# Optimization experiments

Hardware: AMD Instinct MI355X
Metric: run time of the kernel (lower is better)

## Reference

```python
import jax, jax.numpy as jnp
import numpy as np

EPS = 1e-12  # matches torch F.normalize default eps


def _l2norm(x):
    n = jnp.linalg.norm(x, axis=-1, keepdims=True)
    return x / jnp.maximum(n, EPS)


def setup_inputs() -> dict:
    key = jax.random.key(0)
    k1, k2 = jax.random.split(key)
    B, Na, T, Nv, D = 16, 128, 10, 196, 256
    audio_feats = jax.random.normal(k1, (B, Na, D), dtype=jnp.float32)
    visual_feats = jax.random.normal(k2, (B, T, Nv, D), dtype=jnp.float32)
    temperature = jnp.asarray(2.0, dtype=jnp.float32)
    return {"audio_feats": audio_feats, "visual_feats": visual_feats,
            "temperature": temperature}


def reference(audio_feats, visual_feats, temperature):
    # audio_feats: (B, Na, D); visual_feats: (B, T, Nv, D)
    a = _l2norm(audio_feats)                         # (B, Na, D)
    v = _l2norm(visual_feats)                        # (B, T, Nv, D)
    # all-pairs token-level cosine sims: (Bx, By, Na, T, Nv)
    sims = jnp.einsum('xad,ytvd->xyatv', a, v) / temperature
    # aggregate: max over patches, mean over time, mean over audio tokens
    clip_sims = sims.max(axis=-1).mean(axis=-1).mean(axis=-1)  # (B, B)

    # InfoNCE on diagonal
    B = clip_sims.shape[0]
    diag = jnp.arange(B)
    log_p_a2v = jax.nn.log_softmax(clip_sims, axis=1)
    log_p_v2a = jax.nn.log_softmax(clip_sims.T, axis=1)
    losses = -(log_p_a2v[diag, diag] + log_p_v2a[diag, diag])
    contrastive_loss = 0.5 * losses.mean()

    # regularization: non-negativity pressure + temperature band [1, 3]
    neg = jnp.minimum(sims, 0.0)
    l_nonneg = jnp.mean(neg * neg)
    log_t = jnp.log(temperature)
    temp_low = jnp.maximum(-log_t, 0.0) ** 4
    temp_high = jnp.maximum(log_t - jnp.log(3.0), 0.0) ** 4
    reg_loss = l_nonneg + temp_low + temp_high

    total_loss = contrastive_loss + 0.3 * reg_loss
    return (total_loss, contrastive_loss, reg_loss)
```

## Files before the change

### kernel.cpp

```cpp
#include <hip/hip_runtime.h>
#include <stdint.h>


typedef __bf16 bf16x8 __attribute__((ext_vector_type(8)));
typedef float  f32x4  __attribute__((ext_vector_type(4)));

#define P_ROWS 2176

#define WS_A_OFF  ((size_t)0)
#define WS_V_OFF  ((size_t)(1u<<20))
#define WS_CP_OFF (WS_V_OFF + (size_t)16*P_ROWS*512)

__device__ __forceinline__ unsigned short f2bf(float f) {
    unsigned b = __float_as_uint(f);
    return (unsigned short)((b + 0x7fffu + ((b >> 16) & 1u)) >> 16);
}
__device__ __forceinline__ int fenc(float f) {
    int i = __float_as_int(f);
    return i >= 0 ? i : (i ^ 0x7fffffff);
}
__device__ __forceinline__ float fdec(int i) {
    return __int_as_float(i >= 0 ? i : (i ^ 0x7fffffff));
}
__device__ __forceinline__ void gld_lds16(const char* g, char* l) {
    __builtin_amdgcn_global_load_lds(
        (const __attribute__((address_space(1))) void*)g,
        (__attribute__((address_space(3))) void*)l, 16, 0, 0);
}

__global__ __launch_bounds__(512) void prep_kernel(const float* __restrict__ audio,
                                                   const float* __restrict__ visual,
                                                   char* __restrict__ ws)
{
    const int wrow = blockIdx.x * 8 + (threadIdx.x >> 6);
    const int lane = threadIdx.x & 63;
    if (wrow < 2048) {
        const float4 v = *(const float4*)(audio + (size_t)wrow * 256 + lane * 4);
        float ss = v.x*v.x + v.y*v.y + v.z*v.z + v.w*v.w;
        #pragma unroll
        for (int m = 1; m < 64; m <<= 1) ss += __shfl_xor(ss, m);
        const float sc = 1.0f / fmaxf(sqrtf(ss), 1e-12f);
        ushort4 o;
        o.x = f2bf(v.x*sc); o.y = f2bf(v.y*sc); o.z = f2bf(v.z*sc); o.w = f2bf(v.w*sc);
        *(ushort4*)(ws + WS_A_OFF + (size_t)wrow * 512 + lane * 8) = o;
    } else {
        const int vr  = wrow - 2048;
        const int y   = vr / P_ROWS;
        const int rem = vr % P_ROWS;
        const int t   = rem / 208;
        const int v   = rem % 208;
        ushort4 o = make_ushort4(0, 0, 0, 0);
        if (t < 10 && v < 196) {
            const float4 f = *(const float4*)(visual + (size_t)((y*10 + t)*196 + v) * 256 + lane * 4);
            float ss = f.x*f.x + f.y*f.y + f.z*f.z + f.w*f.w;
            #pragma unroll
            for (int m = 1; m < 64; m <<= 1) ss += __shfl_xor(ss, m);
            const float sc = 1.0f / fmaxf(sqrtf(ss), 1e-12f);
            o.x = f2bf(f.x*sc); o.y = f2bf(f.y*sc); o.z = f2bf(f.z*sc); o.w = f2bf(f.w*sc);
        }
        const int u   = lane >> 1;
        const int swz = u ^ (vr & 7);
        *(ushort4*)(ws + WS_V_OFF + (size_t)vr * 512 + (swz << 4) + ((lane & 1) << 3)) = o;
    }
}

#define STAGE(c_, buf_) do {                                        \
    const char* s_ = vbase + (size_t)(c_) * 32768 + tid * 16;       \
    char* d_ = &smem[buf_][0] + tid * 16;                           \
    gld_lds16(s_,         d_);                                      \
    gld_lds16(s_ +  8192, d_ +  8192);                              \
    gld_lds16(s_ + 16384, d_ + 16384);                              \
    gld_lds16(s_ + 24576, d_ + 24576);                              \
} while (0)

__global__ __launch_bounds__(512, 4) void main_kernel(char* __restrict__ ws)
{
    __shared__ __align__(16) char smem[2][32768];
    __shared__ int part_lds[640];
    __shared__ float red[16];

    const int tid  = threadIdx.x;
    const int lane = tid & 63;
    const int wid  = tid >> 6;
    const int l15  = lane & 15;
    const int kg   = lane >> 4;
    const int aw   = wid & 3;
    const int vw   = wid >> 2;

    const int b = blockIdx.x;
    const int xcd = b & 7, s = b >> 3;
    const int y = xcd * 2 + (s >> 5);
    const int x = (s >> 1) & 15;
    const int h = s & 1;

    part_lds[tid] = (int)0x80000000;
    if (tid < 128) part_lds[512 + tid] = (int)0x80000000;

    bf16x8 af[2][8];
    {
        const char* ab = ws + WS_A_OFF + (size_t)(x*128 + aw*32) * 512;
        #pragma unroll
        for (int j = 0; j < 2; ++j)
            #pragma unroll
            for (int k = 0; k < 8; ++k) {
                uint4 u = *(const uint4*)(ab + (j*16 + l15)*512 + k*64 + kg*16);
                af[j][k] = __builtin_bit_cast(bf16x8, u);
            }
    }
    asm volatile("s_waitcnt vmcnt(0)" ::: "memory");

    const char* vbase = ws + WS_V_OFF + ((size_t)y * P_ROWS + (size_t)h * 1040) * 512;

    float nn = 0.f;
    float rmax0 = -3.4e38f, rmax1 = -3.4e38f;

    STAGE(0, 0);
    __builtin_amdgcn_s_barrier();

    int cur = 0;
    for (int c = 0; c < 17; ++c) {
        if (c < 16) {
            STAGE(c + 1, cur ^ 1);
            asm volatile("s_waitcnt vmcnt(4)" ::: "memory");
        } else {
            asm volatile("s_waitcnt vmcnt(0)" ::: "memory");
        }
        __builtin_amdgcn_s_barrier();

        #pragma unroll
        for (int q2 = 0; q2 < 2; ++q2) {
            const int f = 4*c + 2*vw + q2;
            if (f < 65) {
                const int qq = 2*vw + q2;
                const char* bb = &smem[cur][0] + (qq*16 + l15) * 512;
                const int sw = (l15 & 7) << 4;

                f32x4 acc0 = {0.f,0.f,0.f,0.f}, acc1 = {0.f,0.f,0.f,0.f};
                bf16x8 vf[4];
                #pragma unroll
                for (int k = 0; k < 4; ++k) {
                    uint4 q = *(const uint4*)(bb + ((((k*4 + kg) << 4)) ^ sw));
                    vf[k] = __builtin_bit_cast(bf16x8, q);
                }
                #pragma unroll
                for (int k = 0; k < 4; ++k) {
                    acc0 = __builtin_amdgcn_mfma_f32_16x16x32_bf16(vf[k], af[0][k], acc0, 0,0,0);
                    acc1 = __builtin_amdgcn_mfma_f32_16x16x32_bf16(vf[k], af[1][k], acc1, 0,0,0);
                }
                #pragma unroll
                for (int k = 0; k < 4; ++k) {
                    uint4 q = *(const uint4*)(bb + (((k*4 + 16 + kg) << 4) ^ sw));
                    vf[k] = __builtin_bit_cast(bf16x8, q);
                }
                #pragma unroll
                for (int k = 0; k < 4; ++k) {
                    acc0 = __builtin_amdgcn_mfma_f32_16x16x32_bf16(vf[k], af[0][k+4], acc0, 0,0,0);
                    acc1 = __builtin_amdgcn_mfma_f32_16x16x32_bf16(vf[k], af[1][k+4], acc1, 0,0,0);
                }

                const int t  = f / 13;
                const int ft = f - t*13;
                float m0 = fmaxf(fmaxf(acc0[0], acc0[1]), fmaxf(acc0[2], acc0[3]));
                float m1 = fmaxf(fmaxf(acc1[0], acc1[1]), fmaxf(acc1[2], acc1[3]));
                #pragma unroll
                for (int i = 0; i < 4; ++i) {
                    const float g0 = fminf(acc0[i], 0.f);
                    const float g1 = fminf(acc1[i], 0.f);
                    nn = fmaf(g0, g0, nn);
                    nn = fmaf(g1, g1, nn);
                }
                if (ft == 12 && kg != 0) { m0 = -3.4e38f; m1 = -3.4e38f; }
                rmax0 = fmaxf(rmax0, m0);
                rmax1 = fmaxf(rmax1, m1);

                const int fn = q2 ? f + 3 : f + 1;
                const int tn = (fn < 65) ? fn / 13 : 5;
                if (tn != t) {
                    float v0 = fmaxf(rmax0, __shfl_xor(rmax0, 16));
                    v0 = fmaxf(v0, __shfl_xor(v0, 32));
                    float v1 = fmaxf(rmax1, __shfl_xor(rmax1, 16));
                    v1 = fmaxf(v1, __shfl_xor(v1, 32));
                    if (lane < 16) {
                        atomicMax(&part_lds[(aw*32 + l15) * 5 + t],      fenc(v0));
                        atomicMax(&part_lds[(aw*32 + 16 + l15) * 5 + t], fenc(v1));
                    }
                    rmax0 = -3.4e38f;
                    rmax1 = -3.4e38f;
                }
            }
        }
        asm volatile("" ::: "memory");
        __builtin_amdgcn_s_barrier();
        cur ^= 1;
    }

    __syncthreads();

    float sum = 0.f;
    for (int i = tid; i < 640; i += 512) sum += fdec(part_lds[i]);
    #pragma unroll
    for (int m = 32; m >= 1; m >>= 1) {
        sum += __shfl_xor(sum, m);
        nn  += __shfl_xor(nn, m);
    }
    if (lane == 0) { red[wid] = sum; red[8 + wid] = nn; }
    __syncthreads();
    if (tid == 0) {
        float S = 0.f, N = 0.f;
        #pragma unroll
        for (int w = 0; w < 8; ++w) { S += red[w]; N += red[8 + w]; }
        float* cp = (float*)(ws + WS_CP_OFF);
        cp[(x*16 + y)*2 + h]       = S;
        cp[512 + (x*16 + y)*2 + h] = N;
    }
}

__global__ void final_kernel(const char* __restrict__ ws,
                             const float* __restrict__ temp,
                             float* __restrict__ out)
{
    __shared__ float cs[16][17];
    __shared__ float nnred[256];
    __shared__ float lse_r[16], lse_c[16];
    const int tid = threadIdx.x;
    const float T = temp[0];
    const float* cp = (const float*)(ws + WS_CP_OFF);
    cs[tid >> 4][tid & 15] = (cp[tid*2] + cp[tid*2 + 1]) / (1280.0f * T);
    nnred[tid] = cp[512 + tid*2] + cp[512 + tid*2 + 1];
    __syncthreads();
    for (int s = 128; s > 0; s >>= 1) {
        if (tid < s) nnred[tid] += nnred[tid + s];
        __syncthreads();
    }
    if (tid < 16) {
        float m = -3.4e38f;
        for (int j = 0; j < 16; ++j) m = fmaxf(m, cs[tid][j]);
        float s = 0.f;
        for (int j = 0; j < 16; ++j) s += expf(cs[tid][j] - m);
        lse_r[tid] = m + logf(s);
    } else if (tid < 32) {
        const int c = tid - 16;
        float m = -3.4e38f;
        for (int j = 0; j < 16; ++j) m = fmaxf(m, cs[j][c]);
        float s = 0.f;
        for (int j = 0; j < 16; ++j) s += expf(cs[j][c] - m);
        lse_c[c] = m + logf(s);
    }
    __syncthreads();
    if (tid == 0) {
        float acc = 0.f;
        for (int i = 0; i < 16; ++i)
            acc += (lse_r[i] - cs[i][i]) + (lse_c[i] - cs[i][i]);
        const float contrastive = 0.5f * acc * (1.0f / 16.0f);
        const float l_nonneg = nnred[0] / (64225280.0f * T * T);
        const float lt = logf(T);
        float tl = fmaxf(-lt, 0.f); tl = tl * tl; tl = tl * tl;
        float th = fmaxf(lt - 1.0986122886681098f, 0.f); th = th * th; th = th * th;
        const float reg = l_nonneg + tl + th;
        out[0] = contrastive + 0.3f * reg;
        out[1] = contrastive;
        out[2] = reg;
    }
}

extern "C" void kernel_launch(void* const* d_in, const int* in_sizes, int n_in,
                              void* d_out, int out_size, void* d_ws, size_t ws_size,
                              hipStream_t stream)
{
    const float* audio  = (const float*)d_in[0];
    const float* visual = (const float*)d_in[1];
    const float* temp   = (const float*)d_in[2];
    char* ws = (char*)d_ws;

    prep_kernel<<<4608, 512, 0, stream>>>(audio, visual, ws);
    main_kernel<<<512, 512, 0, stream>>>(ws);
    final_kernel<<<1, 256, 0, stream>>>(ws, temp, (float*)d_out);
}
```

Measured before the change: 126.7 us.

## Switch main GEMM to 32x32x16 MFMA with 256-row padded visual tiles

```diff
diff --git a/kernel.cpp b/kernel.cpp
--- a/kernel.cpp
+++ b/kernel.cpp
@@ -3,18 +3,14 @@
 
 
 typedef __bf16 bf16x8 __attribute__((ext_vector_type(8)));
-typedef float  f32x4  __attribute__((ext_vector_type(4)));
-
-#define P_ROWS 2176
+typedef float  f32x16 __attribute__((ext_vector_type(16)));
 
 #define WS_A_OFF  ((size_t)0)
 #define WS_V_OFF  ((size_t)(1u<<20))
-#define WS_CP_OFF (WS_V_OFF + (size_t)16*P_ROWS*512)
-
-__device__ __forceinline__ unsigned short f2bf(float f) {
-    unsigned b = __float_as_uint(f);
-    return (unsigned short)((b + 0x7fffu + ((b >> 16) & 1u)) >> 16);
-}
+#define WS_CP_OFF (WS_V_OFF + (size_t)16*2560*512)
+
+#define NINF (-3.4e38f)
+
 __device__ __forceinline__ int fenc(float f) {
     int i = __float_as_int(f);
     return i >= 0 ? i : (i ^ 0x7fffffff);
@@ -28,187 +24,197 @@
         (__attribute__((address_space(3))) void*)l, 16, 0, 0);
 }
 
-__global__ __launch_bounds__(512) void prep_kernel(const float* __restrict__ audio,
+__global__ __launch_bounds__(256) void prep_kernel(const float* __restrict__ audio,
                                                    const float* __restrict__ visual,
                                                    char* __restrict__ ws)
 {
-    const int wrow = blockIdx.x * 8 + (threadIdx.x >> 6);
+    const int wave = blockIdx.x * 4 + (threadIdx.x >> 6);
     const int lane = threadIdx.x & 63;
-    if (wrow < 2048) {
-        const float4 v = *(const float4*)(audio + (size_t)wrow * 256 + lane * 4);
-        float ss = v.x*v.x + v.y*v.y + v.z*v.z + v.w*v.w;
-        #pragma unroll
-        for (int m = 1; m < 64; m <<= 1) ss += __shfl_xor(ss, m);
-        const float sc = 1.0f / fmaxf(sqrtf(ss), 1e-12f);
-        ushort4 o;
-        o.x = f2bf(v.x*sc); o.y = f2bf(v.y*sc); o.z = f2bf(v.z*sc); o.w = f2bf(v.w*sc);
-        *(ushort4*)(ws + WS_A_OFF + (size_t)wrow * 512 + lane * 8) = o;
+    const int g    = lane >> 4;
+    const int sub  = lane & 15;
+    const int row  = wave * 4 + g;
+
+    float4 v0 = {0,0,0,0}, v1 = {0,0,0,0}, v2 = {0,0,0,0}, v3 = {0,0,0,0};
+    size_t dst0, dst1;
+    if (row < 2048) {
+        const float* s = audio + (size_t)row * 256 + sub * 16;
+        v0 = *(const float4*)(s);  v1 = *(const float4*)(s + 4);
+        v2 = *(const float4*)(s + 8); v3 = *(const float4*)(s + 12);
+        dst0 = WS_A_OFF + (size_t)row * 512 + sub * 32;
+        dst1 = dst0 + 16;
     } else {
-        const int vr  = wrow - 2048;
-        const int y   = vr / P_ROWS;
-        const int rem = vr % P_ROWS;
-        const int t   = rem / 208;
-        const int v   = rem % 208;
-        ushort4 o = make_ushort4(0, 0, 0, 0);
-        if (t < 10 && v < 196) {
-            const float4 f = *(const float4*)(visual + (size_t)((y*10 + t)*196 + v) * 256 + lane * 4);
-            float ss = f.x*f.x + f.y*f.y + f.z*f.z + f.w*f.w;
-            #pragma unroll
-            for (int m = 1; m < 64; m <<= 1) ss += __shfl_xor(ss, m);
-            const float sc = 1.0f / fmaxf(sqrtf(ss), 1e-12f);
-            o.x = f2bf(f.x*sc); o.y = f2bf(f.y*sc); o.z = f2bf(f.z*sc); o.w = f2bf(f.w*sc);
-        }
-        const int u   = lane >> 1;
-        const int swz = u ^ (vr & 7);
-        *(ushort4*)(ws + WS_V_OFF + (size_t)vr * 512 + (swz << 4) + ((lane & 1) << 3)) = o;
-    }
-}
-
-#define STAGE(c_, buf_) do {                                        \
-    const char* s_ = vbase + (size_t)(c_) * 32768 + tid * 16;       \
-    char* d_ = &smem[buf_][0] + tid * 16;                           \
-    gld_lds16(s_,         d_);                                      \
-    gld_lds16(s_ +  8192, d_ +  8192);                              \
-    gld_lds16(s_ + 16384, d_ + 16384);                              \
-    gld_lds16(s_ + 24576, d_ + 24576);                              \
+        const int vr  = row - 2048;
+        const int y   = vr / 2560;
+        const int rem = vr - y * 2560;
+        const int t   = rem >> 8;
+        const int vv  = rem & 255;
+        if (vv < 196) {
+            const float* s = visual + (size_t)((y*10 + t)*196 + vv) * 256 + sub * 16;
+            v0 = *(const float4*)(s);  v1 = *(const float4*)(s + 4);
+            v2 = *(const float4*)(s + 8); v3 = *(const float4*)(s + 12);
+        }
+        const size_t base = WS_V_OFF + (size_t)vr * 512;
+        const int u0 = (2*sub)     ^ (vr & 7);
+        const int u1 = (2*sub + 1) ^ (vr & 7);
+        dst0 = base + ((size_t)u0 << 4);
+        dst1 = base + ((size_t)u1 << 4);
+    }
+
+    float ss = v0.x*v0.x + v0.y*v0.y + v0.z*v0.z + v0.w*v0.w
+             + v1.x*v1.x + v1.y*v1.y + v1.z*v1.z + v1.w*v1.w
+             + v2.x*v2.x + v2.y*v2.y + v2.z*v2.z + v2.w*v2.w
+             + v3.x*v3.x + v3.y*v3.y + v3.z*v3.z + v3.w*v3.w;
+    #pragma unroll
+    for (int m = 1; m < 16; m <<= 1) ss += __shfl_xor(ss, m);
+    const float sc = 1.0f / fmaxf(sqrtf(ss), 1e-12f);
+
+    bf16x8 oa, ob;
+    oa[0]=(__bf16)(v0.x*sc); oa[1]=(__bf16)(v0.y*sc); oa[2]=(__bf16)(v0.z*sc); oa[3]=(__bf16)(v0.w*sc);
+    oa[4]=(__bf16)(v1.x*sc); oa[5]=(__bf16)(v1.y*sc); oa[6]=(__bf16)(v1.z*sc); oa[7]=(__bf16)(v1.w*sc);
+    ob[0]=(__bf16)(v2.x*sc); ob[1]=(__bf16)(v2.y*sc); ob[2]=(__bf16)(v2.z*sc); ob[3]=(__bf16)(v2.w*sc);
+    ob[4]=(__bf16)(v3.x*sc); ob[5]=(__bf16)(v3.y*sc); ob[6]=(__bf16)(v3.z*sc); ob[7]=(__bf16)(v3.w*sc);
+    *(uint4*)(ws + dst0) = __builtin_bit_cast(uint4, oa);
+    *(uint4*)(ws + dst1) = __builtin_bit_cast(uint4, ob);
+}
+
+#define STAGE(c_, buf_) do {                                          \
+    const char* s_ = vbase + (size_t)(c_) * 32768 + tid * 16;         \
+    char* d_ = smem + ((buf_) << 15) + tid * 16;                      \
+    gld_lds16(s_,         d_);         gld_lds16(s_ +  4096, d_ +  4096); \
+    gld_lds16(s_ +  8192, d_ +  8192); gld_lds16(s_ + 12288, d_ + 12288); \
+    gld_lds16(s_ + 16384, d_ + 16384); gld_lds16(s_ + 20480, d_ + 20480); \
+    gld_lds16(s_ + 24576, d_ + 24576); gld_lds16(s_ + 28672, d_ + 28672); \
 } while (0)
 
-__global__ __launch_bounds__(512, 4) void main_kernel(char* __restrict__ ws)
-{
-    __shared__ __align__(16) char smem[2][32768];
+__global__ __launch_bounds__(256, 2) void main_kernel(char* __restrict__ ws)
+{
+    extern __shared__ __align__(16) char smem[];
     __shared__ int part_lds[640];
-    __shared__ float red[16];
+    __shared__ float red[8];
 
     const int tid  = threadIdx.x;
     const int lane = tid & 63;
     const int wid  = tid >> 6;
-    const int l15  = lane & 15;
-    const int kg   = lane >> 4;
-    const int aw   = wid & 3;
-    const int vw   = wid >> 2;
+    const int aw   = wid & 1;
+    const int vw   = wid >> 1;
+    const int l31  = lane & 31;
+    const int hi   = lane >> 5;
 
     const int b = blockIdx.x;
-    const int xcd = b & 7, s = b >> 3;
-    const int y = xcd * 2 + (s >> 5);
-    const int x = (s >> 1) & 15;
-    const int h = s & 1;
-
-    part_lds[tid] = (int)0x80000000;
-    if (tid < 128) part_lds[512 + tid] = (int)0x80000000;
-
-    bf16x8 af[2][8];
+    const int xcd = b & 7, slot = b >> 3;
+    const int y = xcd * 2 + (slot >> 5);
+    const int x = (slot >> 1) & 15;
+    const int h = slot & 1;
+
+    for (int i = tid; i < 640; i += 256) part_lds[i] = (int)0x80000000;
+
+    bf16x8 af0[16], af1[16];
     {
-        const char* ab = ws + WS_A_OFF + (size_t)(x*128 + aw*32) * 512;
+        const char* ab = ws + WS_A_OFF + (size_t)(x*128 + aw*64) * 512;
         #pragma unroll
-        for (int j = 0; j < 2; ++j)
-            #pragma unroll
-            for (int k = 0; k < 8; ++k) {
-                uint4 u = *(const uint4*)(ab + (j*16 + l15)*512 + k*64 + kg*16);
-                af[j][k] = __builtin_bit_cast(bf16x8, u);
-            }
+        for (int k = 0; k < 16; ++k) {
+            af0[k] = __builtin_bit_cast(bf16x8,
+                *(const uint4*)(ab + l31*512 + k*32 + hi*16));
+            af1[k] = __builtin_bit_cast(bf16x8,
+                *(const uint4*)(ab + (32 + l31)*512 + k*32 + hi*16));
+        }
     }
     asm volatile("s_waitcnt vmcnt(0)" ::: "memory");
 
-    const char* vbase = ws + WS_V_OFF + ((size_t)y * P_ROWS + (size_t)h * 1040) * 512;
-
-    float nn = 0.f;
-    float rmax0 = -3.4e38f, rmax1 = -3.4e38f;
+    const char* vbase = ws + WS_V_OFF + ((size_t)y * 2560 + (size_t)h * 1280) * 512;
+
+    float nn = 0.f, rmax0 = NINF, rmax1 = NINF;
 
     STAGE(0, 0);
-    __builtin_amdgcn_s_barrier();
-
-    int cur = 0;
-    for (int c = 0; c < 17; ++c) {
-        if (c < 16) {
-            STAGE(c + 1, cur ^ 1);
-            asm volatile("s_waitcnt vmcnt(4)" ::: "memory");
+
+    for (int c = 0; c < 20; ++c) {
+        if (c < 19) {
+            STAGE(c + 1, (c + 1) & 1);
+            asm volatile("s_waitcnt vmcnt(8)" ::: "memory");
         } else {
             asm volatile("s_waitcnt vmcnt(0)" ::: "memory");
         }
         __builtin_amdgcn_s_barrier();
 
-        #pragma unroll
-        for (int q2 = 0; q2 < 2; ++q2) {
-            const int f = 4*c + 2*vw + q2;
-            if (f < 65) {
-                const int qq = 2*vw + q2;
-                const char* bb = &smem[cur][0] + (qq*16 + l15) * 512;
-                const int sw = (l15 & 7) << 4;
-
-                f32x4 acc0 = {0.f,0.f,0.f,0.f}, acc1 = {0.f,0.f,0.f,0.f};
-                bf16x8 vf[4];
+        const int f  = 2*c + vw;
+        const int ft = f & 7;
+        if (ft != 7) {
+            const char* bb = smem + ((c & 1) << 15) + ((vw*32 + l31) * 512);
+            const int sx = (l31 & 7) << 4;
+
+            f32x16 acc0 = {}, acc1 = {};
+            #pragma unroll
+            for (int hf = 0; hf < 2; ++hf) {
+                bf16x8 vf[8];
                 #pragma unroll
-                for (int k = 0; k < 4; ++k) {
-                    uint4 q = *(const uint4*)(bb + ((((k*4 + kg) << 4)) ^ sw));
-                    vf[k] = __builtin_bit_cast(bf16x8, q);
+                for (int k8 = 0; k8 < 8; ++k8) {
+                    const int u = (((hf*8 + k8)*2 + hi) << 4) ^ sx;
+                    vf[k8] = __builtin_bit_cast(bf16x8, *(const uint4*)(bb + u));
                 }
                 #pragma unroll
-                for (int k = 0; k < 4; ++k) {
-                    acc0 = __builtin_amdgcn_mfma_f32_16x16x32_bf16(vf[k], af[0][k], acc0, 0,0,0);
-                    acc1 = __builtin_amdgcn_mfma_f32_16x16x32_bf16(vf[k], af[1][k], acc1, 0,0,0);
+                for (int k8 = 0; k8 < 8; ++k8) {
+                    acc0 = __builtin_amdgcn_mfma_f32_32x32x16_bf16(vf[k8], af0[hf*8 + k8], acc0, 0,0,0);
+                    acc1 = __builtin_amdgcn_mfma_f32_32x32x16_bf16(vf[k8], af1[hf*8 + k8], acc1, 0,0,0);
                 }
-                #pragma unroll
-                for (int k = 0; k < 4; ++k) {
-                    uint4 q = *(const uint4*)(bb + (((k*4 + 16 + kg) << 4) ^ sw));
-                    vf[k] = __builtin_bit_cast(bf16x8, q);
-                }
-                #pragma unroll
-                for (int k = 0; k < 4; ++k) {
-                    acc0 = __builtin_amdgcn_mfma_f32_16x16x32_bf16(vf[k], af[0][k+4], acc0, 0,0,0);
-                    acc1 = __builtin_amdgcn_mfma_f32_16x16x32_bf16(vf[k], af[1][k+4], acc1, 0,0,0);
-                }
-
-                const int t  = f / 13;
-                const int ft = f - t*13;
-                float m0 = fmaxf(fmaxf(acc0[0], acc0[1]), fmaxf(acc0[2], acc0[3]));
-                float m1 = fmaxf(fmaxf(acc1[0], acc1[1]), fmaxf(acc1[2], acc1[3]));
-                #pragma unroll
-                for (int i = 0; i < 4; ++i) {
-                    const float g0 = fminf(acc0[i], 0.f);
-                    const float g1 = fminf(acc1[i], 0.f);
-                    nn = fmaf(g0, g0, nn);
-                    nn = fmaf(g1, g1, nn);
-                }
-                if (ft == 12 && kg != 0) { m0 = -3.4e38f; m1 = -3.4e38f; }
-                rmax0 = fmaxf(rmax0, m0);
-                rmax1 = fmaxf(rmax1, m1);
-
-                const int fn = q2 ? f + 3 : f + 1;
-                const int tn = (fn < 65) ? fn / 13 : 5;
-                if (tn != t) {
-                    float v0 = fmaxf(rmax0, __shfl_xor(rmax0, 16));
-                    v0 = fmaxf(v0, __shfl_xor(v0, 32));
-                    float v1 = fmaxf(rmax1, __shfl_xor(rmax1, 16));
-                    v1 = fmaxf(v1, __shfl_xor(v1, 32));
-                    if (lane < 16) {
-                        atomicMax(&part_lds[(aw*32 + l15) * 5 + t],      fenc(v0));
-                        atomicMax(&part_lds[(aw*32 + 16 + l15) * 5 + t], fenc(v1));
-                    }
-                    rmax0 = -3.4e38f;
-                    rmax1 = -3.4e38f;
-                }
-            }
+            }
+
+            #pragma unroll
+            for (int i = 0; i < 16; ++i) {
+                const float g0 = fminf(acc0[i], 0.f);
+                const float g1 = fminf(acc1[i], 0.f);
+                nn = fmaf(g0, g0, nn);
+                nn = fmaf(g1, g1, nn);
+            }
+            float m0, m1;
+            if (ft == 6) {
+                m0 = fmaxf(fmaxf(acc0[0], acc0[1]), fmaxf(acc0[2], acc0[3]));
+                m1 = fmaxf(fmaxf(acc1[0], acc1[1]), fmaxf(acc1[2], acc1[3]));
+                if (hi) { m0 = NINF; m1 = NINF; }
+            } else {
+                float a0 = fmaxf(fmaxf(acc0[0], acc0[1]), fmaxf(acc0[2], acc0[3]));
+                float a1 = fmaxf(fmaxf(acc0[4], acc0[5]), fmaxf(acc0[6], acc0[7]));
+                float a2 = fmaxf(fmaxf(acc0[8], acc0[9]), fmaxf(acc0[10], acc0[11]));
+                float a3 = fmaxf(fmaxf(acc0[12], acc0[13]), fmaxf(acc0[14], acc0[15]));
+                m0 = fmaxf(fmaxf(a0, a1), fmaxf(a2, a3));
+                float b0 = fmaxf(fmaxf(acc1[0], acc1[1]), fmaxf(acc1[2], acc1[3]));
+                float b1 = fmaxf(fmaxf(acc1[4], acc1[5]), fmaxf(acc1[6], acc1[7]));
+                float b2 = fmaxf(fmaxf(acc1[8], acc1[9]), fmaxf(acc1[10], acc1[11]));
+                float b3 = fmaxf(fmaxf(acc1[12], acc1[13]), fmaxf(acc1[14], acc1[15]));
+                m1 = fmaxf(fmaxf(b0, b1), fmaxf(b2, b3));
+            }
+            rmax0 = fmaxf(rmax0, m0);
+            rmax1 = fmaxf(rmax1, m1);
+        }
+
+        if ((c & 3) == 3) {
+            const int tl = c >> 2;
+            float vv0 = fmaxf(rmax0, __shfl_xor(rmax0, 32));
+            float vv1 = fmaxf(rmax1, __shfl_xor(rmax1, 32));
+            if (hi == 0) {
+                atomicMax(&part_lds[(aw*64 + l31) * 5 + tl],      fenc(vv0));
+                atomicMax(&part_lds[(aw*64 + 32 + l31) * 5 + tl], fenc(vv1));
+            }
+            rmax0 = NINF; rmax1 = NINF;
         }
         asm volatile("" ::: "memory");
         __builtin_amdgcn_s_barrier();
-        cur ^= 1;
     }
 
     __syncthreads();
 
     float sum = 0.f;
-    for (int i = tid; i < 640; i += 512) sum += fdec(part_lds[i]);
+    for (int i = tid; i < 640; i += 256) sum += fdec(part_lds[i]);
     #pragma unroll
-    for (int m = 32; m >= 1; m >>= 1) {
+    for (int m = 1; m < 64; m <<= 1) {
         sum += __shfl_xor(sum, m);
         nn  += __shfl_xor(nn, m);
     }
-    if (lane == 0) { red[wid] = sum; red[8 + wid] = nn; }
+    if (lane == 0) { red[wid] = sum; red[4 + wid] = nn; }
     __syncthreads();
     if (tid == 0) {
         float S = 0.f, N = 0.f;
         #pragma unroll
-        for (int w = 0; w < 8; ++w) { S += red[w]; N += red[8 + w]; }
+        for (int w = 0; w < 4; ++w) { S += red[w]; N += red[4 + w]; }
         float* cp = (float*)(ws + WS_CP_OFF);
         cp[(x*16 + y)*2 + h]       = S;
         cp[512 + (x*16 + y)*2 + h] = N;
@@ -233,14 +239,14 @@
         __syncthreads();
     }
     if (tid < 16) {
-        float m = -3.4e38f;
+        float m = NINF;
         for (int j = 0; j < 16; ++j) m = fmaxf(m, cs[tid][j]);
         float s = 0.f;
         for (int j = 0; j < 16; ++j) s += expf(cs[tid][j] - m);
         lse_r[tid] = m + logf(s);
     } else if (tid < 32) {
         const int c = tid - 16;
-        float m = -3.4e38f;
+        float m = NINF;
         for (int j = 0; j < 16; ++j) m = fmaxf(m, cs[j][c]);
         float s = 0.f;
         for (int j = 0; j < 16; ++j) s += expf(cs[j][c] - m);
@@ -272,7 +278,7 @@
     const float* temp   = (const float*)d_in[2];
     char* ws = (char*)d_ws;
 
-    prep_kernel<<<4608, 512, 0, stream>>>(audio, visual, ws);
-    main_kernel<<<512, 512, 0, stream>>>(ws);
+    prep_kernel<<<2688, 256, 0, stream>>>(audio, visual, ws);
+    main_kernel<<<512, 256, 65536, stream>>>(ws);
     final_kernel<<<1, 256, 0, stream>>>(ws, temp, (float*)d_out);
 }
```

Result: no change. 128.4 us (+1.4%).
